# Performance work log

Measured on AMD Instinct MI355X. Metric: run time of the kernel, lower is better.

Reference implementation:

```python
import jax, jax.numpy as jnp
import numpy as np

SEQ, EMB, QKV = 4096, 1024, 1024

def setup_inputs() -> dict:
    key = jax.random.key(0)
    k_x, k_q, k_k, k_v = jax.random.split(key, 4)
    scale = 1.0 / np.sqrt(EMB)
    return {
        "x": jax.random.normal(k_x, (SEQ, EMB), dtype=jnp.float32),
        "W_q": jax.random.normal(k_q, (EMB, QKV), dtype=jnp.float32) * scale,
        "W_k": jax.random.normal(k_k, (EMB, QKV), dtype=jnp.float32) * scale,
        "W_v": jax.random.normal(k_v, (EMB, QKV), dtype=jnp.float32) * scale,
    }

def reference(x, W_q, W_k, W_v):
    # Single-head scaled dot-product attention, unbatched: x [S, E]
    d_k = W_q.shape[1]
    Q = x @ W_q          # [S, D]
    K = x @ W_k          # [S, D]
    V = x @ W_v          # [S, D]
    scores = (Q @ K.T) * (1.0 / jnp.sqrt(jnp.asarray(d_k, dtype=x.dtype)))  # [S, S]
    attn = jax.nn.softmax(scores, axis=-1)
    return attn @ V      # [S, D]
```

## Files before the change

### kernel.cpp

```cpp
#include <hip/hip_runtime.h>
#include <cstdint>

#define S_DIM 4096
#define E_DIM 1024
#define D_DIM 1024

typedef __bf16 bf16x8 __attribute__((ext_vector_type(8)));
typedef float  f32x4  __attribute__((ext_vector_type(4)));
typedef unsigned short u16x8 __attribute__((ext_vector_type(8)));

__device__ __forceinline__ unsigned short f2bf(float f) {
  unsigned u = __float_as_uint(f);
  unsigned r = (u + 0x7fffu + ((u >> 16) & 1u)) >> 16;
  return (unsigned short)r;
}

__device__ __forceinline__ void lds_copy16(const unsigned short* g, const unsigned short* l) {
  auto gp = reinterpret_cast<__attribute__((address_space(1))) unsigned int*>(
      reinterpret_cast<uintptr_t>(g));
  auto lp = reinterpret_cast<__attribute__((address_space(3))) unsigned int*>(
      reinterpret_cast<uintptr_t>(l));
  __builtin_amdgcn_global_load_lds(gp, lp, 16, 0, 0);
}

__global__ __launch_bounds__(256) void prep_kernel(
    const float* __restrict__ x,
    const float* __restrict__ Wq, const float* __restrict__ Wk, const float* __restrict__ Wv,
    unsigned short* __restrict__ xbf, unsigned short* __restrict__ Wt,
    float* __restrict__ lsum) {
  const int z = blockIdx.z;
  const int tid = threadIdx.x;
  if (z < 3) {
    const float* W = (z == 0) ? Wq : (z == 1 ? Wk : Wv);
    unsigned short* out = Wt + (size_t)z * E_DIM * D_DIM;
    __shared__ unsigned short tile[32][33];
    int bc = blockIdx.x * 32, br = blockIdx.y * 32;
    int tx = tid & 31, ty = tid >> 5;
#pragma unroll
    for (int i = 0; i < 32; i += 8)
      tile[ty + i][tx] = f2bf(W[(size_t)(br + ty + i) * D_DIM + bc + tx]);
    __syncthreads();
#pragma unroll
    for (int i = 0; i < 32; i += 8)
      out[(size_t)(bc + ty + i) * E_DIM + br + tx] = tile[tx][ty + i];
  } else {
    int bid = blockIdx.y * 32 + blockIdx.x;
    int i = (bid * 256 + tid) * 16;
#pragma unroll
    for (int h = 0; h < 2; h++) {
      float4 a = *(const float4*)(x + i + h * 8);
      float4 b = *(const float4*)(x + i + h * 8 + 4);
      u16x8 o;
      o[0] = f2bf(a.x); o[1] = f2bf(a.y); o[2] = f2bf(a.z); o[3] = f2bf(a.w);
      o[4] = f2bf(b.x); o[5] = f2bf(b.y); o[6] = f2bf(b.z); o[7] = f2bf(b.w);
      *(u16x8*)(xbf + i + h * 8) = o;
    }
    if (bid < 16) lsum[bid * 256 + tid] = 0.f;
  }
}

__global__ __launch_bounds__(256) void transpose_bf16_kernel(
    const unsigned short* __restrict__ in, unsigned short* __restrict__ out,
    int ldin, int ldout) {
  __shared__ unsigned short tile[32][33];
  int bc = blockIdx.x * 32, br = blockIdx.y * 32;
  int tx = threadIdx.x & 31, ty = threadIdx.x >> 5;
#pragma unroll
  for (int i = 0; i < 32; i += 8)
    tile[ty + i][tx] = in[(size_t)(br + ty + i) * ldin + bc + tx];
  __syncthreads();
#pragma unroll
  for (int i = 0; i < 32; i += 8)
    out[(size_t)(bc + ty + i) * ldout + br + tx] = tile[tx][ty + i];
}

template <int MODE, bool SPLIT3>
__global__ __launch_bounds__(256, 2) void gemm_bt_kernel(
    const unsigned short* __restrict__ A, int lda,
    const unsigned short* __restrict__ Bt, int ldb,
    void* __restrict__ Cp, unsigned short* __restrict__ C1,
    unsigned short* __restrict__ C2, int ldc,
    int Kper, float scale, float* __restrict__ lsum) {
  __shared__ __align__(16) unsigned short sA[128 * 64];
  __shared__ __align__(16) unsigned short sB[128 * 64];

  const int tid = threadIdx.x;

  int flat = blockIdx.y * gridDim.x + blockIdx.x;
  int numInG = 8 * gridDim.x;
  int g = flat / numInG;
  int r = flat - g * numInG;
  const int bm = (g * 8 + (r & 7)) * 128;
  const int bn = (r >> 3) * 128;

  const int wave = tid >> 6;
  const int lane = tid & 63;
  const int q    = lane >> 4;
  const int l16  = lane & 15;
  const int wm   = (wave >> 1) * 64;
  const int wn   = (wave & 1) * 64;

  f32x4 zero = {0.f, 0.f, 0.f, 0.f};
  f32x4 acc[4][4];
#pragma unroll
  for (int t = 0; t < 4; t++)
#pragma unroll
    for (int u = 0; u < 4; u++) acc[t][u] = zero;

  const int srow   = tid >> 3;
  const int schunk = (tid & 7) ^ (srow & 3);
  const int kbase  = blockIdx.z * Kper;
  const unsigned short* ap = A  + (size_t)(bm + srow) * lda + kbase + schunk * 8;
  const unsigned short* bp = Bt + (size_t)(bn + srow) * ldb + kbase + schunk * 8;
  unsigned short* saw = sA + wave * 512;
  unsigned short* sbw = sB + wave * 512;
  const size_t stepA = (size_t)32 * lda;
  const size_t stepB = (size_t)32 * ldb;

  const int sw = (q ^ (l16 & 3)) * 8;

  for (int k0 = 0; k0 < Kper; k0 += 64) {
#pragma unroll
    for (int p = 0; p < 4; p++) {
      lds_copy16(ap + k0 + p * stepA, saw + p * 2048);
      lds_copy16(bp + k0 + p * stepB, sbw + p * 2048);
    }
    __syncthreads();

#pragma unroll
    for (int h = 0; h < 2; h++) {
      bf16x8 af[4], bfv[4];
#pragma unroll
      for (int t = 0; t < 4; t++)
        af[t] = *reinterpret_cast<const bf16x8*>(sA + (wm + t * 16 + l16) * 64 + h * 32 + sw);
#pragma unroll
      for (int u = 0; u < 4; u++)
        bfv[u] = *reinterpret_cast<const bf16x8*>(sB + (wn + u * 16 + l16) * 64 + h * 32 + sw);
#pragma unroll
      for (int t = 0; t < 4; t++)
#pragma unroll
        for (int u = 0; u < 4; u++)
          acc[t][u] = __builtin_amdgcn_mfma_f32_16x16x32_bf16(af[t], bfv[u], acc[t][u], 0, 0, 0);
    }
    __syncthreads();
  }

  unsigned short* cb16 = (unsigned short*)Cp;
  int coloff = bn;
  if constexpr (SPLIT3) {
    int which = bn >> 10;
    cb16 = (which == 0) ? (unsigned short*)Cp : (which == 1 ? C1 : C2);
    coloff = bn & 1023;
  }

#pragma unroll
  for (int t = 0; t < 4; t++) {
#pragma unroll
    for (int rr = 0; rr < 4; rr++) {
      const int row = bm + wm + t * 16 + q * 4 + rr;
      float invl = 1.0f;
      if constexpr (MODE == 2) invl = 1.0f / lsum[row];
      float rs = 0.f;
#pragma unroll
      for (int u = 0; u < 4; u++) {
        const int col = coloff + wn + u * 16 + l16;
        float v = acc[t][u][rr] * scale;
        if constexpr (MODE == 0) {
          cb16[(size_t)row * ldc + col] = f2bf(v);
        } else if constexpr (MODE == 1) {
          float p = __expf(v - 8.0f);
          rs += p;
          cb16[(size_t)row * ldc + col] = f2bf(p);
        } else {
          unsafeAtomicAdd((float*)Cp + (size_t)row * ldc + col, acc[t][u][rr] * invl);
        }
      }
      if constexpr (MODE == 1) {
        rs += __shfl_xor(rs, 1);
        rs += __shfl_xor(rs, 2);
        rs += __shfl_xor(rs, 4);
        rs += __shfl_xor(rs, 8);
        if (l16 == 0) unsafeAtomicAdd(&lsum[row], rs);
      }
    }
  }
}

extern "C" void kernel_launch(void* const* d_in, const int* in_sizes, int n_in,
                              void* d_out, int out_size, void* d_ws, size_t ws_size,
                              hipStream_t stream) {
  const float* x  = (const float*)d_in[0];
  const float* Wq = (const float*)d_in[1];
  const float* Wk = (const float*)d_in[2];
  const float* Wv = (const float*)d_in[3];
  float* out = (float*)d_out;

  char* ws = (char*)d_ws;
  const size_t MB = 1024 * 1024;
  unsigned short* SP   = (unsigned short*)(ws);
  unsigned short* Vtmp = (unsigned short*)(ws);
  unsigned short* xbf  = (unsigned short*)(ws + 8 * MB);
  unsigned short* Wt   = (unsigned short*)(ws + 16 * MB);
  unsigned short* Qbf  = (unsigned short*)(ws + 32 * MB);
  unsigned short* Kbf  = (unsigned short*)(ws + 40 * MB);
  unsigned short* Vt   = (unsigned short*)(ws + 48 * MB);
  float*          lsum = (float*)(ws + 56 * MB);

  dim3 blk(256);

  dim3 prgrid(32, 32, 4);
  prep_kernel<<<prgrid, blk, 0, stream>>>(x, Wq, Wk, Wv, xbf, Wt, lsum);

  dim3 pgrid(24, 32, 1);
  gemm_bt_kernel<0, true><<<pgrid, blk, 0, stream>>>(
      xbf, E_DIM, Wt, E_DIM, Qbf, Kbf, Vtmp, D_DIM, E_DIM, 1.0f, nullptr);

  dim3 vtgrid(32, 128);
  transpose_bf16_kernel<<<vtgrid, blk, 0, stream>>>(Vtmp, Vt, D_DIM, S_DIM);

  dim3 sgrid(32, 32, 1);
  gemm_bt_kernel<1, false><<<sgrid, blk, 0, stream>>>(
      Qbf, D_DIM, Kbf, D_DIM, SP, nullptr, nullptr, S_DIM, D_DIM, 0.03125f, lsum);

  hipMemsetAsync(out, 0, (size_t)S_DIM * D_DIM * sizeof(float), stream);
  dim3 ogrid(8, 32, 2);
  gemm_bt_kernel<2, false><<<ogrid, blk, 0, stream>>>(
      SP, S_DIM, Vt, S_DIM, out, nullptr, nullptr, D_DIM, S_DIM / 2, 1.0f, lsum);
}
```

Measured before the change: 224.2 us.

## Fuse projection, scores and PV GEMMs into one persistent kernel with grid barriers

```diff
diff --git a/kernel.cpp b/kernel.cpp
--- a/kernel.cpp
+++ b/kernel.cpp
@@ -23,11 +23,24 @@
   __builtin_amdgcn_global_load_lds(gp, lp, 16, 0, 0);
 }
 
+__device__ __forceinline__ void dev_barrier(unsigned int* ctr, unsigned int target) {
+  __threadfence();
+  __syncthreads();
+  if (threadIdx.x == 0) {
+    atomicAdd(ctr, 1u);
+    while (__hip_atomic_load(ctr, __ATOMIC_RELAXED, __HIP_MEMORY_SCOPE_AGENT) < target) {
+      __builtin_amdgcn_s_sleep(2);
+    }
+  }
+  __syncthreads();
+  __threadfence();
+}
+
 __global__ __launch_bounds__(256) void prep_kernel(
     const float* __restrict__ x,
     const float* __restrict__ Wq, const float* __restrict__ Wk, const float* __restrict__ Wv,
     unsigned short* __restrict__ xbf, unsigned short* __restrict__ Wt,
-    float* __restrict__ lsum) {
+    float* __restrict__ lsum, unsigned int* __restrict__ bar) {
   const int z = blockIdx.z;
   const int tid = threadIdx.x;
   if (z < 3) {
@@ -56,47 +69,23 @@
       *(u16x8*)(xbf + i + h * 8) = o;
     }
     if (bid < 16) lsum[bid * 256 + tid] = 0.f;
-  }
-}
-
-__global__ __launch_bounds__(256) void transpose_bf16_kernel(
-    const unsigned short* __restrict__ in, unsigned short* __restrict__ out,
-    int ldin, int ldout) {
-  __shared__ unsigned short tile[32][33];
-  int bc = blockIdx.x * 32, br = blockIdx.y * 32;
-  int tx = threadIdx.x & 31, ty = threadIdx.x >> 5;
-#pragma unroll
-  for (int i = 0; i < 32; i += 8)
-    tile[ty + i][tx] = in[(size_t)(br + ty + i) * ldin + bc + tx];
-  __syncthreads();
-#pragma unroll
-  for (int i = 0; i < 32; i += 8)
-    out[(size_t)(bc + ty + i) * ldout + br + tx] = tile[tx][ty + i];
-}
-
-template <int MODE, bool SPLIT3>
-__global__ __launch_bounds__(256, 2) void gemm_bt_kernel(
-    const unsigned short* __restrict__ A, int lda,
-    const unsigned short* __restrict__ Bt, int ldb,
-    void* __restrict__ Cp, unsigned short* __restrict__ C1,
-    unsigned short* __restrict__ C2, int ldc,
-    int Kper, float scale, float* __restrict__ lsum) {
-  __shared__ __align__(16) unsigned short sA[128 * 64];
-  __shared__ __align__(16) unsigned short sB[128 * 64];
-
+    if (bid == 0 && tid < 8) bar[tid] = 0u;
+  }
+}
+
+template <int MODE, int NSPLIT>
+__device__ __forceinline__ void gemm_body(
+    const unsigned short* A, int lda,
+    const unsigned short* Bt, int ldb,
+    void* Cp, unsigned short* C1, int ldc,
+    int Kper, float scale, float* lsum,
+    int bm, int bn, unsigned short* sA, unsigned short* sB) {
   const int tid = threadIdx.x;
-
-  int flat = blockIdx.y * gridDim.x + blockIdx.x;
-  int numInG = 8 * gridDim.x;
-  int g = flat / numInG;
-  int r = flat - g * numInG;
-  const int bm = (g * 8 + (r & 7)) * 128;
-  const int bn = (r >> 3) * 128;
-
   const int wave = tid >> 6;
   const int lane = tid & 63;
   const int q    = lane >> 4;
   const int l16  = lane & 15;
+  const int lx   = l16 & 7;
   const int wm   = (wave >> 1) * 64;
   const int wn   = (wave & 1) * 64;
 
@@ -108,17 +97,14 @@
     for (int u = 0; u < 4; u++) acc[t][u] = zero;
 
   const int srow   = tid >> 3;
-  const int schunk = (tid & 7) ^ (srow & 3);
-  const int kbase  = blockIdx.z * Kper;
-  const unsigned short* ap = A  + (size_t)(bm + srow) * lda + kbase + schunk * 8;
-  const unsigned short* bp = Bt + (size_t)(bn + srow) * ldb + kbase + schunk * 8;
+  const int schunk = (tid & 7) ^ (srow & 7);
+  const unsigned short* ap = A  + (size_t)(bm + srow) * lda + schunk * 8;
+  const unsigned short* bp = Bt + (size_t)(bn + srow) * ldb + schunk * 8;
   unsigned short* saw = sA + wave * 512;
   unsigned short* sbw = sB + wave * 512;
   const size_t stepA = (size_t)32 * lda;
   const size_t stepB = (size_t)32 * ldb;
 
-  const int sw = (q ^ (l16 & 3)) * 8;
-
   for (int k0 = 0; k0 < Kper; k0 += 64) {
 #pragma unroll
     for (int p = 0; p < 4; p++) {
@@ -130,12 +116,13 @@
 #pragma unroll
     for (int h = 0; h < 2; h++) {
       bf16x8 af[4], bfv[4];
+      const int pc = (((h << 2) | q) ^ lx) * 8;
 #pragma unroll
       for (int t = 0; t < 4; t++)
-        af[t] = *reinterpret_cast<const bf16x8*>(sA + (wm + t * 16 + l16) * 64 + h * 32 + sw);
+        af[t] = *reinterpret_cast<const bf16x8*>(sA + (wm + t * 16 + l16) * 64 + pc);
 #pragma unroll
       for (int u = 0; u < 4; u++)
-        bfv[u] = *reinterpret_cast<const bf16x8*>(sB + (wn + u * 16 + l16) * 64 + h * 32 + sw);
+        bfv[u] = *reinterpret_cast<const bf16x8*>(sB + (wn + u * 16 + l16) * 64 + pc);
 #pragma unroll
       for (int t = 0; t < 4; t++)
 #pragma unroll
@@ -147,19 +134,17 @@
 
   unsigned short* cb16 = (unsigned short*)Cp;
   int coloff = bn;
-  if constexpr (SPLIT3) {
-    int which = bn >> 10;
-    cb16 = (which == 0) ? (unsigned short*)Cp : (which == 1 ? C1 : C2);
+  if constexpr (NSPLIT == 2) {
+    if (bn >= 1024) cb16 = C1;
     coloff = bn & 1023;
   }
+  float* o32 = (float*)Cp;
 
 #pragma unroll
   for (int t = 0; t < 4; t++) {
 #pragma unroll
     for (int rr = 0; rr < 4; rr++) {
       const int row = bm + wm + t * 16 + q * 4 + rr;
-      float invl = 1.0f;
-      if constexpr (MODE == 2) invl = 1.0f / lsum[row];
       float rs = 0.f;
 #pragma unroll
       for (int u = 0; u < 4; u++) {
@@ -172,7 +157,7 @@
           rs += p;
           cb16[(size_t)row * ldc + col] = f2bf(p);
         } else {
-          unsafeAtomicAdd((float*)Cp + (size_t)row * ldc + col, acc[t][u][rr] * invl);
+          o32[(size_t)row * ldc + col] = v;
         }
       }
       if constexpr (MODE == 1) {
@@ -186,6 +171,69 @@
   }
 }
 
+__global__ __launch_bounds__(256, 2) void fused_kernel(
+    unsigned short* xbf, unsigned short* Wt,
+    unsigned short* Qbf, unsigned short* Kbf, unsigned short* Vt,
+    unsigned short* SP, float* lsum, float* Prt, float* out,
+    unsigned int* bar) {
+  __shared__ __align__(16) unsigned short lds[16384];
+  unsigned short* sA = lds;
+  unsigned short* sB = lds + 8192;
+  const int bid = blockIdx.x;
+  const int tid = threadIdx.x;
+
+  {
+    const int g = bid >> 7, r = bid & 127;
+    gemm_body<0, 2>(xbf, E_DIM, Wt, E_DIM, Qbf, Kbf, D_DIM,
+                    E_DIM, 1.0f, nullptr, (g * 8 + (r & 7)) * 128, (r >> 3) * 128,
+                    sA, sB);
+    if (bid < 256) {
+      gemm_body<0, 1>(Wt + 2 * E_DIM * D_DIM, E_DIM, xbf, E_DIM, Vt, nullptr, S_DIM,
+                      E_DIM, 1.0f, nullptr, (bid & 7) * 128, (bid >> 3) * 128,
+                      sA, sB);
+    }
+  }
+  dev_barrier(bar + 0, gridDim.x);
+
+#pragma unroll 1
+  for (int it = 0; it < 2; ++it) {
+    const int idx = bid + it * 512;
+    const int g = idx >> 8, r = idx & 255;
+    gemm_body<1, 1>(Qbf, D_DIM, Kbf, D_DIM, SP, nullptr, S_DIM,
+                    D_DIM, 0.03125f, lsum, (g * 8 + (r & 7)) * 128, (r >> 3) * 128,
+                    sA, sB);
+  }
+  dev_barrier(bar + 1, gridDim.x);
+
+  {
+    const int ot = bid >> 1, kh = bid & 1;
+    float* dst = kh ? out : Prt;
+    gemm_body<2, 1>(SP + kh * 2048, S_DIM, Vt + kh * 2048, S_DIM, dst, nullptr,
+                    D_DIM, 2048, 1.0f, nullptr, (ot & 31) * 128, (ot >> 5) * 128,
+                    sA, sB);
+  }
+  dev_barrier(bar + 2, gridDim.x);
+
+  {
+    const float4* p0 = (const float4*)Prt;
+    float4* po = (float4*)out;
+    const int base = bid * 2048 + tid;
+#pragma unroll
+    for (int i = 0; i < 8; ++i) {
+      const int v = base + i * 256;
+      const float inv = 1.0f / lsum[v >> 8];
+      float4 a = po[v];
+      float4 b = p0[v];
+      float4 o;
+      o.x = (a.x + b.x) * inv;
+      o.y = (a.y + b.y) * inv;
+      o.z = (a.z + b.z) * inv;
+      o.w = (a.w + b.w) * inv;
+      po[v] = o;
+    }
+  }
+}
+
 extern "C" void kernel_launch(void* const* d_in, const int* in_sizes, int n_in,
                               void* d_out, int out_size, void* d_ws, size_t ws_size,
                               hipStream_t stream) {
@@ -198,32 +246,20 @@
   char* ws = (char*)d_ws;
   const size_t MB = 1024 * 1024;
   unsigned short* SP   = (unsigned short*)(ws);
-  unsigned short* Vtmp = (unsigned short*)(ws);
   unsigned short* xbf  = (unsigned short*)(ws + 8 * MB);
   unsigned short* Wt   = (unsigned short*)(ws + 16 * MB);
   unsigned short* Qbf  = (unsigned short*)(ws + 32 * MB);
   unsigned short* Kbf  = (unsigned short*)(ws + 40 * MB);
   unsigned short* Vt   = (unsigned short*)(ws + 48 * MB);
+  float*          Prt  = (float*)(ws + 32 * MB);
   float*          lsum = (float*)(ws + 56 * MB);
+  unsigned int*   bar  = (unsigned int*)(ws + 56 * MB + 16 * 1024);
 
   dim3 blk(256);
 
   dim3 prgrid(32, 32, 4);
-  prep_kernel<<<prgrid, blk, 0, stream>>>(x, Wq, Wk, Wv, xbf, Wt, lsum);
-
-  dim3 pgrid(24, 32, 1);
-  gemm_bt_kernel<0, true><<<pgrid, blk, 0, stream>>>(
-      xbf, E_DIM, Wt, E_DIM, Qbf, Kbf, Vtmp, D_DIM, E_DIM, 1.0f, nullptr);
-
-  dim3 vtgrid(32, 128);
-  transpose_bf16_kernel<<<vtgrid, blk, 0, stream>>>(Vtmp, Vt, D_DIM, S_DIM);
-
-  dim3 sgrid(32, 32, 1);
-  gemm_bt_kernel<1, false><<<sgrid, blk, 0, stream>>>(
-      Qbf, D_DIM, Kbf, D_DIM, SP, nullptr, nullptr, S_DIM, D_DIM, 0.03125f, lsum);
-
-  hipMemsetAsync(out, 0, (size_t)S_DIM * D_DIM * sizeof(float), stream);
-  dim3 ogrid(8, 32, 2);
-  gemm_bt_kernel<2, false><<<ogrid, blk, 0, stream>>>(
-      SP, S_DIM, Vt, S_DIM, out, nullptr, nullptr, D_DIM, S_DIM / 2, 1.0f, lsum);
-}
+  prep_kernel<<<prgrid, blk, 0, stream>>>(x, Wq, Wk, Wv, xbf, Wt, lsum, bar);
+
+  fused_kernel<<<dim3(512), blk, 0, stream>>>(
+      xbf, Wt, Qbf, Kbf, Vt, SP, lsum, Prt, out, bar);
+}
```

Measured after the change: 584.9 us. 161% more time.
